# Optimization experiments

Hardware: AMD Instinct MI355X
Metric: run time of the kernel (lower is better)

The kernel has to match this reference:

```python
import jax, jax.numpy as jnp
import numpy as np

H = 512  # all four hidden sizes
P_DROP = 0.5


def _lstm_cell(x, h, c, w_ih, w_hh, b_ih, b_hh):
    # gates: [B, 4H]; order i, f, g, o (torch LSTMCell convention)
    gates = x @ w_ih.T + b_ih + h @ w_hh.T + b_hh
    i, f, g, o = jnp.split(gates, 4, axis=-1)
    c_new = jax.nn.sigmoid(f) * c + jax.nn.sigmoid(i) * jnp.tanh(g)
    h_new = jax.nn.sigmoid(o) * jnp.tanh(c_new)
    return h_new, c_new


def setup_inputs() -> dict:
    key = jax.random.key(0)
    ks = jax.random.split(key, 20)
    B, T = 128, 512
    s = 1.0 / np.sqrt(H)
    inp = {"input": jax.random.normal(ks[0], (B, T), dtype=jnp.float32)}
    in_sizes = [1, H, H, H]
    for l in range(4):
        k0, k1, k2, k3 = jax.random.split(ks[1 + l], 4)
        inp[f"w_ih{l+1}"] = jax.random.uniform(k0, (4 * H, in_sizes[l]), jnp.float32, -s, s)
        inp[f"w_hh{l+1}"] = jax.random.uniform(k1, (4 * H, H), jnp.float32, -s, s)
        inp[f"b_ih{l+1}"] = jax.random.uniform(k2, (4 * H,), jnp.float32, -s, s)
        inp[f"b_hh{l+1}"] = jax.random.uniform(k3, (4 * H,), jnp.float32, -s, s)
    inp["w_lin"] = jax.random.uniform(ks[10], (1, H), jnp.float32, -s, s)
    inp["b_lin"] = jax.random.uniform(ks[11], (1,), jnp.float32, -s, s)
    return inp


def reference(input, w_ih1, w_hh1, b_ih1, b_hh1,
              w_ih2, w_hh2, b_ih2, b_hh2,
              w_ih3, w_hh3, b_ih3, b_hh3,
              w_ih4, w_hh4, b_ih4, b_hh4,
              w_lin, b_lin):
    B, T = input.shape
    # dropout masks, fixed key (training=True dropout, p=0.5, scale 1/(1-p)=2)
    mkey = jax.random.key(42)
    mk = jax.random.split(mkey, 4)
    masks = tuple(
        jax.random.bernoulli(mk[l], 1.0 - P_DROP, (T, B, H)).astype(input.dtype) * 2.0
        for l in range(4)
    )
    xs = (input.T[:, :, None],) + masks  # x_t: [T, B, 1]

    z = jnp.zeros((B, H), dtype=input.dtype)
    init = (z, z, z, z, z, z, z, z)

    def step(carry, xt):
        h1, c1, h2, c2, h3, c3, h4, c4 = carry
        x, m1, m2, m3, m4 = xt
        h1, c1 = _lstm_cell(x, h1, c1, w_ih1, w_hh1, b_ih1, b_hh1)
        h1 = h1 * m1  # dropped h is also the recurrent state (as in source)
        h2, c2 = _lstm_cell(h1, h2, c2, w_ih2, w_hh2, b_ih2, b_hh2)
        h2 = h2 * m2
        h3, c3 = _lstm_cell(h2, h3, c3, w_ih3, w_hh3, b_ih3, b_hh3)
        h3 = h3 * m3
        h4, c4 = _lstm_cell(h3, h4, c4, w_ih4, w_hh4, b_ih4, b_hh4)
        h4 = h4 * m4
        out = h4 @ w_lin.T + b_lin  # [B, 1]
        return (h1, c1, h2, c2, h3, c3, h4, c4), out

    _, ys = jax.lax.scan(step, init, xs)  # ys: [T, B, 1]
    return jnp.transpose(ys, (1, 0, 2))[..., 0]  # [B, T]
```

## Files before the change

kernel.cpp:

```cpp
#include <hip/hip_runtime.h>
#include <cstdint>

#define TT 512

typedef float f32x16 __attribute__((ext_vector_type(16)));
typedef short s16x8 __attribute__((ext_vector_type(8)));
typedef _Float16 f16x8 __attribute__((ext_vector_type(8)));

__host__ __device__ inline void tf2x32(uint32_t k0, uint32_t k1, uint32_t& x0, uint32_t& x1) {
  uint32_t k2 = k0 ^ k1 ^ 0x1BD11BDAu;
#define TF_R(r) { x0 += x1; x1 = (x1 << r) | (x1 >> (32 - r)); x1 ^= x0; }
  x0 += k0; x1 += k1;
  TF_R(13) TF_R(15) TF_R(26) TF_R(6)
  x0 += k1; x1 += k2 + 1u;
  TF_R(17) TF_R(29) TF_R(16) TF_R(24)
  x0 += k2; x1 += k0 + 2u;
  TF_R(13) TF_R(15) TF_R(26) TF_R(6)
  x0 += k0; x1 += k1 + 3u;
  TF_R(17) TF_R(29) TF_R(16) TF_R(24)
  x0 += k1; x1 += k2 + 4u;
  TF_R(13) TF_R(15) TF_R(26) TF_R(6)
  x0 += k2; x1 += k0 + 5u;
#undef TF_R
}

struct KParams {
  const float* input;
  const float* w_ih[4];
  const float* w_hh[4];
  const float* b_ih[4];
  const float* b_hh[4];
  const float* w_lin;
  const float* b_lin;
  unsigned short* hbuf;
  uint32_t* cnt;
  float* out;
  uint32_t mk[4][2];
};

__device__ __forceinline__ unsigned short f2h(float v) {
  _Float16 h = (_Float16)v;
  return __builtin_bit_cast(unsigned short, h);
}
__device__ __forceinline__ float sigm(float x) { return 1.f / (1.f + __expf(-x)); }
__device__ __forceinline__ float tanh_fast(float x) {
  float a = fabsf(x);
  float e = __expf(-2.f * a);
  float r = (1.f - e) / (1.f + e);
  return copysignf(r, x);
}

#define MFMA16(A, B, C) __builtin_amdgcn_mfma_f32_32x32x16_f16((A), (B), (C), 0, 0, 0)

__device__ __forceinline__ void vmwait_dyn(int a) {
  switch (a) {
    case 0: asm volatile("s_waitcnt vmcnt(0)" ::: "memory"); break;
    case 1: asm volatile("s_waitcnt vmcnt(2)" ::: "memory"); break;
    case 2: asm volatile("s_waitcnt vmcnt(4)" ::: "memory"); break;
    case 3: asm volatile("s_waitcnt vmcnt(6)" ::: "memory"); break;
    case 4: asm volatile("s_waitcnt vmcnt(8)" ::: "memory"); break;
    case 5: asm volatile("s_waitcnt vmcnt(10)" ::: "memory"); break;
    case 6: asm volatile("s_waitcnt vmcnt(12)" ::: "memory"); break;
    default: asm volatile("s_waitcnt vmcnt(14)" ::: "memory"); break;
  }
  __builtin_amdgcn_sched_barrier(0);
}

#define ISSUE2(s0, s1, ptr) \
  asm volatile("global_load_dwordx4 %0, %2, off sc0 sc1\n\t" \
               "global_load_dwordx4 %1, %2, off offset:1024 sc0 sc1" \
               : "=&v"(s0), "=&v"(s1) : "v"(ptr) : "memory")

template <int FRAGBASE>
__device__ __forceinline__ void gemm8(const unsigned short* buf,
                                      const f16x8 (&W)[2][16],
                                      int wave, int lane,
                                      f32x16& a00, f32x16& a01, f32x16& a10, f32x16& a11) {
  s16x8 st[8][2];
  const int lofs = wave * 1024 + lane * 8;
#pragma unroll
  for (int i = 0; i < 8; ++i) {
    const unsigned short* p = buf + i * 4096 + lofs;
    ISSUE2(st[i][0], st[i][1], p);
  }
#pragma unroll
  for (int i = 0; i < 8; ++i) {
    vmwait_dyn(7 - i);
    f16x8 b0 = __builtin_bit_cast(f16x8, st[i][0]);
    f16x8 b1 = __builtin_bit_cast(f16x8, st[i][1]);
    a00 = MFMA16(W[0][FRAGBASE + i], b0, a00);
    a10 = MFMA16(W[1][FRAGBASE + i], b0, a10);
    a01 = MFMA16(W[0][FRAGBASE + i], b1, a01);
    a11 = MFMA16(W[1][FRAGBASE + i], b1, a11);
  }
}

__device__ __forceinline__ void pollcnt(const uint32_t* p, uint32_t tgt, bool slp) {
  while (__hip_atomic_load(p, __ATOMIC_RELAXED, __HIP_MEMORY_SCOPE_AGENT) < tgt) {
    if (slp) __builtin_amdgcn_s_sleep(1);
  }
}
__device__ __forceinline__ uint32_t tgt_of(int T) { return 32u * ((uint32_t)(T >> 3) + 1u); }

__global__ __launch_bounds__(256, 1) void lstm4(KParams P) {
  const int wg   = blockIdx.x;
  const int grp  = wg & 7;
  const int iwg  = wg >> 3;
  const int l    = grp >> 1;
  const int p    = grp & 1;
  const int tid  = threadIdx.x;
  const int wave = tid >> 6;
  const int lane = tid & 63;

  __shared__ float part[4][64][64];
  __shared__ float bias_s[64];
  __shared__ float wih1_s[64];
  __shared__ float wlin_s[16];
  __shared__ float red_s[4][64];

#define CNT(kind, g, slot) (P.cnt + (((kind) * 8 + (g)) * 8 + (slot)) * 32)

  f16x8 W[2][16];
  {
#pragma unroll
    for (int ji = 0; ji < 16; ++ji) {
      const bool valid = (l > 0) || (ji < 8);
      const float* wsrc = (l == 0 || ji >= 8) ? P.w_hh[l] : P.w_ih[l];
      const int blk = (ji & 7) * 4 + wave;
      const int col = blk * 16 + (lane >> 5) * 8;
#pragma unroll
      for (int m = 0; m < 2; ++m) {
        const int rl = m * 32 + (lane & 31);
        const int grow = (rl >> 4) * 512 + iwg * 16 + (rl & 15);
        f16x8 v8 = {0, 0, 0, 0, 0, 0, 0, 0};
        if (valid) {
          const float* s = wsrc + grow * 512 + col;
#pragma unroll
          for (int e = 0; e < 8; ++e) v8[e] = (_Float16)s[e];
        }
        W[m][ji] = v8;
      }
    }
  }
  if (tid < 64) {
    const int rl = tid;
    const int grow = (rl >> 4) * 512 + iwg * 16 + (rl & 15);
    bias_s[rl] = P.b_ih[l][grow] + P.b_hh[l][grow];
    wih1_s[rl] = (l == 0) ? P.w_ih[0][grow] : 0.f;
  }
  if (l == 3 && tid < 16) wlin_s[tid] = P.w_lin[iwg * 16 + tid];
  __syncthreads();

  const int gb = p * 64 + lane;
  const uint32_t kk0 = P.mk[l][0], kk1 = P.mk[l][1];
  float cst[4] = {0.f, 0.f, 0.f, 0.f};

  float fac[4];
#pragma unroll
  for (int cc = 0; cc < 4; ++cc) {
    const int gu = iwg * 16 + wave * 4 + cc;
    uint32_t j = (uint32_t)gb * 512u + (uint32_t)gu;
    uint32_t x0 = 0u, x1 = j;
    tf2x32(kk0, kk1, x0, x1);
    fac[cc] = ((x0 ^ x1) & 0x80000000u) ? 0.f : 2.f;
  }

  for (int t = 0; t < TT; ++t) {
    float xin = 0.f;
    if (l == 0) xin = P.input[gb * 512 + t];

    f32x16 a00 = {0,0,0,0,0,0,0,0,0,0,0,0,0,0,0,0};
    f32x16 a01 = {0,0,0,0,0,0,0,0,0,0,0,0,0,0,0,0};
    f32x16 a10 = {0,0,0,0,0,0,0,0,0,0,0,0,0,0,0,0};
    f32x16 a11 = {0,0,0,0,0,0,0,0,0,0,0,0,0,0,0,0};

    const unsigned short* pB = P.hbuf + (size_t)(((l - 1) * 2 + p) * 2 + (t & 1)) * 32768;
    const unsigned short* pO = P.hbuf + (size_t)(grp * 2 + ((t - 1) & 1)) * 32768;

    if (l > 0) {
      pollcnt(CNT(0, grp - 2, t & 7), tgt_of(t), true);
      asm volatile("s_waitcnt vmcnt(0)" ::: "memory");
      gemm8<0>(pB, W, wave, lane, a00, a01, a10, a11);
    }
    if (t > 0) {
      pollcnt(CNT(0, grp, (t - 1) & 7), tgt_of(t - 1), false);
      asm volatile("s_waitcnt vmcnt(0)" ::: "memory");
      if (l > 0) gemm8<8>(pO, W, wave, lane, a00, a01, a10, a11);
      else       gemm8<0>(pO, W, wave, lane, a00, a01, a10, a11);
    }

#pragma unroll
    for (int r = 0; r < 16; ++r) {
      const int row = (r & 3) + 8 * (r >> 2) + 4 * (lane >> 5);
      const int cl = lane & 31;
      part[wave][row][cl]           = a00[r];
      part[wave][row][32 + cl]      = a01[r];
      part[wave][32 + row][cl]      = a10[r];
      part[wave][32 + row][32 + cl] = a11[r];
    }
    __syncthreads();
    if (tid == 0 && l > 0)
      __hip_atomic_fetch_add(CNT(1, grp, t & 7), 1u, __ATOMIC_RELAXED, __HIP_MEMORY_SCOPE_AGENT);

    float si[4], sf[4], sg[4], so[4];
#pragma unroll
    for (int cc = 0; cc < 4; ++cc) {
      const int ul = wave * 4 + cc;
      si[cc] = part[0][ul][lane]      + part[1][ul][lane]      + part[2][ul][lane]      + part[3][ul][lane];
      sf[cc] = part[0][16 + ul][lane] + part[1][16 + ul][lane] + part[2][16 + ul][lane] + part[3][16 + ul][lane];
      sg[cc] = part[0][32 + ul][lane] + part[1][32 + ul][lane] + part[2][32 + ul][lane] + part[3][32 + ul][lane];
      so[cc] = part[0][48 + ul][lane] + part[1][48 + ul][lane] + part[2][48 + ul][lane] + part[3][48 + ul][lane];
    }

    float osum = 0.f;
    unsigned short hv[4];
#pragma unroll
    for (int cc = 0; cc < 4; ++cc) {
      const int ul = wave * 4 + cc;
      float pi = si[cc] + bias_s[ul];
      float pf = sf[cc] + bias_s[16 + ul];
      float pg = sg[cc] + bias_s[32 + ul];
      float po = so[cc] + bias_s[48 + ul];
      if (l == 0) {
        pi += wih1_s[ul] * xin;
        pf += wih1_s[16 + ul] * xin;
        pg += wih1_s[32 + ul] * xin;
        po += wih1_s[48 + ul] * xin;
      }
      float ig = sigm(pi), fg = sigm(pf), gg = tanh_fast(pg), og = sigm(po);
      float cn = fg * cst[cc] + ig * gg;
      cst[cc] = cn;
      float hh = og * tanh_fast(cn) * fac[cc];
      hv[cc] = f2h(hh);
      if (l == 3) osum += hh * wlin_s[ul];
    }

    if (l < 3 && t >= 2)
      pollcnt(CNT(1, grp + 2, (t - 2) & 7), tgt_of(t - 2), true);

    {
      uint32_t d0 = (uint32_t)hv[0] | ((uint32_t)hv[1] << 16);
      uint32_t d1 = (uint32_t)hv[2] | ((uint32_t)hv[3] << 16);
      typedef uint32_t u32x2 __attribute__((ext_vector_type(2)));
      u32x2 dv = {d0, d1};
      const int elem = ((iwg * 2 + (lane >> 5)) * 64 + (wave >> 1) * 32 + (lane & 31)) * 8 + (wave & 1) * 4;
      unsigned short* wb = P.hbuf + (size_t)(grp * 2 + (t & 1)) * 32768 + elem;
      asm volatile("global_store_dwordx2 %0, %1, off sc0 sc1" :: "v"(wb), "v"(dv) : "memory");
      asm volatile("s_waitcnt vmcnt(0)" ::: "memory");
    }
    __syncthreads();
    if (tid == 0)
      __hip_atomic_fetch_add(CNT(0, grp, t & 7), 1u, __ATOMIC_RELAXED, __HIP_MEMORY_SCOPE_AGENT);

    if (l == 3) {
      red_s[wave][lane] = osum;
      __syncthreads();
      if (tid < 64) {
        float v = red_s[0][tid] + red_s[1][tid] + red_s[2][tid] + red_s[3][tid];
        if (iwg == 0) v += P.b_lin[0];
        atomicAdd(&P.out[(p * 64 + tid) * 512 + t], v);
      }
    }

    if (t + 1 < TT) {
#pragma unroll
      for (int cc = 0; cc < 4; ++cc) {
        const int gu = iwg * 16 + wave * 4 + cc;
        uint32_t j = ((uint32_t)(t + 1) * 128u + (uint32_t)gb) * 512u + (uint32_t)gu;
        uint32_t x0 = 0u, x1 = j;
        tf2x32(kk0, kk1, x0, x1);
        fac[cc] = ((x0 ^ x1) & 0x80000000u) ? 0.f : 2.f;
      }
    }
  }
#undef CNT
}

extern "C" void kernel_launch(void* const* d_in, const int* in_sizes, int n_in,
                              void* d_out, int out_size, void* d_ws, size_t ws_size,
                              hipStream_t stream) {
  (void)in_sizes; (void)n_in; (void)ws_size;
  KParams P;
  P.input = (const float*)d_in[0];
  for (int l = 0; l < 4; ++l) {
    P.w_ih[l] = (const float*)d_in[1 + 4 * l];
    P.w_hh[l] = (const float*)d_in[2 + 4 * l];
    P.b_ih[l] = (const float*)d_in[3 + 4 * l];
    P.b_hh[l] = (const float*)d_in[4 + 4 * l];
  }
  P.w_lin = (const float*)d_in[17];
  P.b_lin = (const float*)d_in[18];
  unsigned char* ws = (unsigned char*)d_ws;
  P.hbuf = (unsigned short*)(ws);
  P.cnt  = (uint32_t*)(ws + (1u << 20));
  P.out  = (float*)d_out;

  for (uint32_t i = 0; i < 4; ++i) {
    uint32_t x0 = 0u, x1 = i;
    tf2x32(0u, 42u, x0, x1);
    P.mk[i][0] = x0; P.mk[i][1] = x1;
  }

  hipMemsetAsync(P.cnt, 0, 2 * 8 * 8 * 32 * sizeof(uint32_t), stream);
  hipMemsetAsync(d_out, 0, (size_t)out_size * sizeof(float), stream);
  hipLaunchKernelGGL(lstm4, dim3(256), dim3(256), 0, stream, P);
}
```

Before: 2.799 ms.

## Overlap input and recurrent h loads and vectorize LDS partial-sum reduction

Splits the gemm into separate load-issue and MFMA phases so that, for layers above the first, the input-layer h loads are issued right after their flag arrives. The recurrent-h loads are issued alongside them if the own-group counter is already satisfied, otherwise the input MFMAs run while waiting on it. This hides global-load latency and the polling wait on the serial step critical path. The LDS partial-sum buffer is also re-laid out as padded f32x4 entries so that writes and the cross-wave reduction use 128-bit LDS accesses. The cost is more live VGPRs from the two staging arrays and more complex control flow.

```diff
diff --git a/kernel.cpp b/kernel.cpp
--- a/kernel.cpp
+++ b/kernel.cpp
@@ -4,8 +4,10 @@
 #define TT 512
 
 typedef float f32x16 __attribute__((ext_vector_type(16)));
+typedef float f32x4 __attribute__((ext_vector_type(4)));
 typedef short s16x8 __attribute__((ext_vector_type(8)));
 typedef _Float16 f16x8 __attribute__((ext_vector_type(8)));
+typedef uint32_t u32x2 __attribute__((ext_vector_type(2)));
 
 __host__ __device__ inline void tf2x32(uint32_t k0, uint32_t k1, uint32_t& x0, uint32_t& x1) {
   uint32_t k2 = k0 ^ k1 ^ 0x1BD11BDAu;
@@ -71,18 +73,30 @@
                "global_load_dwordx4 %1, %2, off offset:1024 sc0 sc1" \
                : "=&v"(s0), "=&v"(s1) : "v"(ptr) : "memory")
 
-template <int FRAGBASE>
-__device__ __forceinline__ void gemm8(const unsigned short* buf,
-                                      const f16x8 (&W)[2][16],
-                                      int wave, int lane,
-                                      f32x16& a00, f32x16& a01, f32x16& a10, f32x16& a11) {
-  s16x8 st[8][2];
-  const int lofs = wave * 1024 + lane * 8;
+__device__ __forceinline__ void issue8(const unsigned short* buf, int lofs, s16x8 (&st)[8][2]) {
 #pragma unroll
   for (int i = 0; i < 8; ++i) {
     const unsigned short* p = buf + i * 4096 + lofs;
     ISSUE2(st[i][0], st[i][1], p);
   }
+}
+template <int FRAGBASE>
+__device__ __forceinline__ void mfma8_nowait(const s16x8 (&st)[8][2], const f16x8 (&W)[2][16],
+                                             f32x16& a00, f32x16& a01, f32x16& a10, f32x16& a11) {
+  __builtin_amdgcn_sched_barrier(0);
+#pragma unroll
+  for (int i = 0; i < 8; ++i) {
+    f16x8 b0 = __builtin_bit_cast(f16x8, st[i][0]);
+    f16x8 b1 = __builtin_bit_cast(f16x8, st[i][1]);
+    a00 = MFMA16(W[0][FRAGBASE + i], b0, a00);
+    a10 = MFMA16(W[1][FRAGBASE + i], b0, a10);
+    a01 = MFMA16(W[0][FRAGBASE + i], b1, a01);
+    a11 = MFMA16(W[1][FRAGBASE + i], b1, a11);
+  }
+}
+template <int FRAGBASE>
+__device__ __forceinline__ void mfma8_counted(const s16x8 (&st)[8][2], const f16x8 (&W)[2][16],
+                                              f32x16& a00, f32x16& a01, f32x16& a10, f32x16& a11) {
 #pragma unroll
   for (int i = 0; i < 8; ++i) {
     vmwait_dyn(7 - i);
@@ -99,6 +113,9 @@
   while (__hip_atomic_load(p, __ATOMIC_RELAXED, __HIP_MEMORY_SCOPE_AGENT) < tgt) {
     if (slp) __builtin_amdgcn_s_sleep(1);
   }
+}
+__device__ __forceinline__ bool samplecnt(const uint32_t* p, uint32_t tgt) {
+  return __hip_atomic_load(p, __ATOMIC_RELAXED, __HIP_MEMORY_SCOPE_AGENT) >= tgt;
 }
 __device__ __forceinline__ uint32_t tgt_of(int T) { return 32u * ((uint32_t)(T >> 3) + 1u); }
 
@@ -111,8 +128,10 @@
   const int tid  = threadIdx.x;
   const int wave = tid >> 6;
   const int lane = tid & 63;
-
-  __shared__ float part[4][64][64];
+  const int cl   = lane & 31;
+  const int hi   = lane >> 5;
+
+  __shared__ f32x4 part2[4][64][17];
   __shared__ float bias_s[64];
   __shared__ float wih1_s[64];
   __shared__ float wlin_s[16];
@@ -127,10 +146,10 @@
       const bool valid = (l > 0) || (ji < 8);
       const float* wsrc = (l == 0 || ji >= 8) ? P.w_hh[l] : P.w_ih[l];
       const int blk = (ji & 7) * 4 + wave;
-      const int col = blk * 16 + (lane >> 5) * 8;
+      const int col = blk * 16 + hi * 8;
 #pragma unroll
       for (int m = 0; m < 2; ++m) {
-        const int rl = m * 32 + (lane & 31);
+        const int rl = m * 32 + cl;
         const int grow = (rl >> 4) * 512 + iwg * 16 + (rl & 15);
         f16x8 v8 = {0, 0, 0, 0, 0, 0, 0, 0};
         if (valid) {
@@ -153,6 +172,8 @@
 
   const int gb = p * 64 + lane;
   const uint32_t kk0 = P.mk[l][0], kk1 = P.mk[l][1];
+  const int lofs = wave * 1024 + lane * 8;
+  const int elem = ((iwg * 2 + hi) * 64 + (wave >> 1) * 32 + cl) * 8 + (wave & 1) * 4;
   float cst[4] = {0.f, 0.f, 0.f, 0.f};
 
   float fac[4];
@@ -165,6 +186,8 @@
     fac[cc] = ((x0 ^ x1) & 0x80000000u) ? 0.f : 2.f;
   }
 
+  s16x8 stB[8][2], stO[8][2];
+
   for (int t = 0; t < TT; ++t) {
     float xin = 0.f;
     if (l == 0) xin = P.input[gb * 512 + t];
@@ -179,48 +202,57 @@
 
     if (l > 0) {
       pollcnt(CNT(0, grp - 2, t & 7), tgt_of(t), true);
-      asm volatile("s_waitcnt vmcnt(0)" ::: "memory");
-      gemm8<0>(pB, W, wave, lane, a00, a01, a10, a11);
-    }
-    if (t > 0) {
+      issue8(pB, lofs, stB);
+      if (t > 0) {
+        if (samplecnt(CNT(0, grp, (t - 1) & 7), tgt_of(t - 1))) {
+          issue8(pO, lofs, stO);
+          mfma8_nowait<0>(stB, W, a00, a01, a10, a11);
+          mfma8_counted<8>(stO, W, a00, a01, a10, a11);
+        } else {
+          mfma8_nowait<0>(stB, W, a00, a01, a10, a11);
+          pollcnt(CNT(0, grp, (t - 1) & 7), tgt_of(t - 1), false);
+          issue8(pO, lofs, stO);
+          mfma8_counted<8>(stO, W, a00, a01, a10, a11);
+        }
+      } else {
+        mfma8_counted<0>(stB, W, a00, a01, a10, a11);
+      }
+    } else if (t > 0) {
       pollcnt(CNT(0, grp, (t - 1) & 7), tgt_of(t - 1), false);
-      asm volatile("s_waitcnt vmcnt(0)" ::: "memory");
-      if (l > 0) gemm8<8>(pO, W, wave, lane, a00, a01, a10, a11);
-      else       gemm8<0>(pO, W, wave, lane, a00, a01, a10, a11);
-    }
-
-#pragma unroll
-    for (int r = 0; r < 16; ++r) {
-      const int row = (r & 3) + 8 * (r >> 2) + 4 * (lane >> 5);
-      const int cl = lane & 31;
-      part[wave][row][cl]           = a00[r];
-      part[wave][row][32 + cl]      = a01[r];
-      part[wave][32 + row][cl]      = a10[r];
-      part[wave][32 + row][32 + cl] = a11[r];
+      issue8(pO, lofs, stO);
+      mfma8_counted<0>(stO, W, a00, a01, a10, a11);
+    }
+
+#pragma unroll
+    for (int rs = 0; rs < 4; ++rs) {
+      f32x4 v00 = {a00[4 * rs], a00[4 * rs + 1], a00[4 * rs + 2], a00[4 * rs + 3]};
+      f32x4 v01 = {a01[4 * rs], a01[4 * rs + 1], a01[4 * rs + 2], a01[4 * rs + 3]};
+      f32x4 v10 = {a10[4 * rs], a10[4 * rs + 1], a10[4 * rs + 2], a10[4 * rs + 3]};
+      f32x4 v11 = {a11[4 * rs], a11[4 * rs + 1], a11[4 * rs + 2], a11[4 * rs + 3]};
+      const int cb = 2 * rs + hi;
+      part2[wave][cl][cb]          = v00;
+      part2[wave][cl + 32][cb]     = v01;
+      part2[wave][cl][8 + cb]      = v10;
+      part2[wave][cl + 32][8 + cb] = v11;
     }
     __syncthreads();
     if (tid == 0 && l > 0)
       __hip_atomic_fetch_add(CNT(1, grp, t & 7), 1u, __ATOMIC_RELAXED, __HIP_MEMORY_SCOPE_AGENT);
 
-    float si[4], sf[4], sg[4], so[4];
+    f32x4 si4 = part2[0][lane][wave]      + part2[1][lane][wave]      + part2[2][lane][wave]      + part2[3][lane][wave];
+    f32x4 sf4 = part2[0][lane][4 + wave]  + part2[1][lane][4 + wave]  + part2[2][lane][4 + wave]  + part2[3][lane][4 + wave];
+    f32x4 sg4 = part2[0][lane][8 + wave]  + part2[1][lane][8 + wave]  + part2[2][lane][8 + wave]  + part2[3][lane][8 + wave];
+    f32x4 so4 = part2[0][lane][12 + wave] + part2[1][lane][12 + wave] + part2[2][lane][12 + wave] + part2[3][lane][12 + wave];
+
+    float osum = 0.f;
+    unsigned short hv[4];
 #pragma unroll
     for (int cc = 0; cc < 4; ++cc) {
       const int ul = wave * 4 + cc;
-      si[cc] = part[0][ul][lane]      + part[1][ul][lane]      + part[2][ul][lane]      + part[3][ul][lane];
-      sf[cc] = part[0][16 + ul][lane] + part[1][16 + ul][lane] + part[2][16 + ul][lane] + part[3][16 + ul][lane];
-      sg[cc] = part[0][32 + ul][lane] + part[1][32 + ul][lane] + part[2][32 + ul][lane] + part[3][32 + ul][lane];
-      so[cc] = part[0][48 + ul][lane] + part[1][48 + ul][lane] + part[2][48 + ul][lane] + part[3][48 + ul][lane];
-    }
-
-    float osum = 0.f;
-    unsigned short hv[4];
-#pragma unroll
-    for (int cc = 0; cc < 4; ++cc) {
-      const int ul = wave * 4 + cc;
-      float pi = si[cc] + bias_s[ul];
-      float pf = sf[cc] + bias_s[16 + ul];
-      float pg = sg[cc] + bias_s[32 + ul];
-      float po = so[cc] + bias_s[48 + ul];
+      float pi = si4[cc] + bias_s[ul];
+      float pf = sf4[cc] + bias_s[16 + ul];
+      float pg = sg4[cc] + bias_s[32 + ul];
+      float po = so4[cc] + bias_s[48 + ul];
       if (l == 0) {
         pi += wih1_s[ul] * xin;
         pf += wih1_s[16 + ul] * xin;
@@ -241,9 +273,7 @@
     {
       uint32_t d0 = (uint32_t)hv[0] | ((uint32_t)hv[1] << 16);
       uint32_t d1 = (uint32_t)hv[2] | ((uint32_t)hv[3] << 16);
-      typedef uint32_t u32x2 __attribute__((ext_vector_type(2)));
       u32x2 dv = {d0, d1};
-      const int elem = ((iwg * 2 + (lane >> 5)) * 64 + (wave >> 1) * 32 + (lane & 31)) * 8 + (wave & 1) * 4;
       unsigned short* wb = P.hbuf + (size_t)(grp * 2 + (t & 1)) * 32768 + elem;
       asm volatile("global_store_dwordx2 %0, %1, off sc0 sc1" :: "v"(wb), "v"(dv) : "memory");
       asm volatile("s_waitcnt vmcnt(0)" ::: "memory");
```

Result: faster. 2.533 ms (-9.5%).
